# Optimization experiments

Measured on AMD Instinct MI355X. Metric: run time of the kernel, lower is better.

## Reference

```python
import jax, jax.numpy as jnp
import numpy as np

B, N, C, H, W = 2, 512, 32, 200, 200
THRESH = 0.05
# BEVCamera: x_range=y_range=(-1,1) -> FoV=2 meters; sh = H/FoVy = 100, sw = W/FoVx = 100
SH = H / 2.0
SW = W / 2.0
LOWPASS = 0.3        # 3DGS low-pass filter added to 2D cov diagonal
ALPHA_MIN = 1.0 / 255.0
ALPHA_MAX = 0.99


def setup_inputs() -> dict:
    key = jax.random.key(0)
    k1, k2, k3, k4 = jax.random.split(key, 4)
    features = jax.random.normal(k1, (B, N, C), dtype=jnp.float32)
    means3D = jax.random.uniform(k2, (B, N, 3), dtype=jnp.float32, minval=-1.0, maxval=1.0)
    # build PSD 3D covariances: Sigma = A A^T + eps*I, store 6 upper-tri entries
    A = 0.05 * jax.random.normal(k3, (B, N, 3, 3), dtype=jnp.float32)
    S = jnp.einsum('bnij,bnkj->bnik', A, A) + 1e-4 * jnp.eye(3, dtype=jnp.float32)
    cov3D = jnp.stack([S[..., 0, 0], S[..., 0, 1], S[..., 0, 2],
                       S[..., 1, 1], S[..., 1, 2], S[..., 2, 2]], axis=-1)
    opacities = jax.random.uniform(k4, (B, N, 1), dtype=jnp.float32)
    return {"features": features, "means3D": means3D, "cov3D": cov3D, "opacities": opacities}


def _render_one(features, means3D, cov3D, op):
    # features [N,C], means3D [N,3], cov3D [N,6] (xx,xy,xz,yy,yz,zz), op [N,1]
    dtype = features.dtype
    opac = op[:, 0]
    opac = jnp.where(opac > THRESH, opac, 0.0)  # masked-out gaussians contribute nothing
    # projmatrix: u = H/2 - sh*y (height), v = W/2 - sw*x (width)
    mu_u = H / 2.0 - SH * means3D[:, 1]
    mu_v = W / 2.0 - SW * means3D[:, 0]
    # 2D covariance from orthographic BEV projection J = [[0,-sh,0],[-sw,0,0]]
    Cuu = SH * SH * cov3D[:, 3] + LOWPASS
    Cvv = SW * SW * cov3D[:, 0] + LOWPASS
    Cuv = SH * SW * cov3D[:, 1]
    det = Cuu * Cvv - Cuv * Cuv
    valid = det > 0.0
    inv_det = jnp.where(valid, 1.0 / jnp.where(valid, det, 1.0), 0.0)
    Iuu = Cvv * inv_det
    Ivv = Cuu * inv_det
    Iuv = -Cuv * inv_det
    opac = jnp.where(valid, opac, 0.0)
    uu = jnp.arange(H, dtype=dtype)
    vv = jnp.arange(W, dtype=dtype)
    du = uu[None, :, None] - mu_u[:, None, None]   # [N,H,1]
    dv = vv[None, None, :] - mu_v[:, None, None]   # [N,1,W]
    power = (-0.5 * (Iuu[:, None, None] * du * du + Ivv[:, None, None] * dv * dv)
             - Iuv[:, None, None] * du * dv)       # [N,H,W]
    alpha = jnp.minimum(ALPHA_MAX, opac[:, None, None] * jnp.exp(jnp.minimum(power, 0.0)))
    alpha = jnp.where((power > 0.0) | (alpha < ALPHA_MIN), 0.0, alpha)
    # front-to-back alpha compositing in gaussian index order (all depths are 0 -> stable sort)
    logt = jnp.log1p(-alpha)                       # [N,H,W]
    T = jnp.exp(jnp.cumsum(logt, axis=0) - logt)   # exclusive transmittance
    w = T * alpha                                  # [N,H,W]
    return jnp.einsum('nhw,nc->chw', w, features)  # bg color is zeros


def reference(features, means3D, cov3D, opacities):
    bev = jax.vmap(_render_one)(features, means3D, cov3D, opacities)  # [B,C,H,W]
    num_gaussians = (opacities[..., 0] > THRESH).astype(jnp.float32).sum(axis=-1).mean()
    return bev, num_gaussians
```

## Files before the change

kernel.cpp:

```cpp
#include <hip/hip_runtime.h>
#include <math.h>

#define B_ 2
#define N_ 512
#define C_ 32
#define H_ 200
#define W_ 200
#define HW_ (H_*W_)
#define THRESH_ 0.05f
#define OUT_BEV (B_*C_*H_*W_)
#define NSEG 8
#define TILES_PER_B 625
#define LOG2E 1.4426950408889634f
#define LN2   0.6931471805599453f

__device__ inline float rlane(float x, int l) {
    return __int_as_float(__builtin_amdgcn_readlane(__float_as_int(x), l));
}

__global__ __launch_bounds__(512, 4) void render_kernel(
    const float* __restrict__ features,
    const float* __restrict__ means3D,
    const float* __restrict__ cov3D,
    const float* __restrict__ opacities,
    float* __restrict__ out)
{
    __shared__ float s_T[NSEG][64];
    __shared__ float s_W[NSEG * 64];
    __shared__ float s_acc[NSEG][NSEG][64];

    int blk = blockIdx.x;
    int tid = threadIdx.x;

    if (blk == B_ * TILES_PER_B) {
        float op0 = opacities[tid];
        float op1 = opacities[N_ + tid];
        int cnt = (op0 > THRESH_ ? 1 : 0) + (op1 > THRESH_ ? 1 : 0);
        for (int off = 32; off > 0; off >>= 1) cnt += __shfl_down(cnt, off);
        int* s_red = (int*)s_W;
        if ((tid & 63) == 0) s_red[tid >> 6] = cnt;
        __syncthreads();
        if (tid == 0) {
            int tot = 0;
            for (int g = 0; g < NSEG; ++g) tot += s_red[g];
            out[OUT_BEV] = (float)tot * 0.5f;
        }
        return;
    }

    int b  = blk / TILES_PER_B;
    int t  = blk - b * TILES_PER_B;
    int tu = t / 25;
    int tv = t - tu * 25;
    int wave = __builtin_amdgcn_readfirstlane(tid >> 6);
    int lane = tid & 63;

    float g_mu_u, g_mu_v, g_a2, g_b2, g_c2, g_op, g_thr2;
    bool ov;
    {
        int i = b * N_ + wave * 64 + lane;
        float x  = means3D[i*3 + 0];
        float y  = means3D[i*3 + 1];
        float c0 = cov3D[i*6 + 0];
        float c1 = cov3D[i*6 + 1];
        float c3 = cov3D[i*6 + 3];
        float op = opacities[i];
        g_mu_u = 100.0f - 100.0f * y;
        g_mu_v = 100.0f - 100.0f * x;
        float Cuu = 10000.0f * c3 + 0.3f;
        float Cvv = 10000.0f * c0 + 0.3f;
        float Cuv = 10000.0f * c1;
        float det = Cuu * Cvv - Cuv * Cuv;
        bool valid = det > 0.0f;
        float opac = (op > THRESH_) ? op : 0.0f;
        if (!valid) opac = 0.0f;
        float inv_det = valid ? (1.0f / det) : 0.0f;
        g_a2 = -0.5f * LOG2E * (Cvv * inv_det);
        g_b2 = -0.5f * LOG2E * (Cuu * inv_det);
        g_c2 =  LOG2E * (Cuv * inv_det);
        g_op = opac;
        float tu0 = (float)(tu * 8), tu1 = tu0 + 7.0f;
        float tv0 = (float)(tv * 8), tv1 = tv0 + 7.0f;
        if (opac > 0.0f) {
            float r2 = log2f(255.0f * opac);
            g_thr2 = -r2;
            float rn = LN2 * r2;
            float du_max = sqrtf(fmaxf(2.0f * rn * Cuu, 0.0f)) + 1.0e-3f;
            float dv_max = sqrtf(fmaxf(2.0f * rn * Cvv, 0.0f)) + 1.0e-3f;
            ov = (g_mu_u - du_max <= tu1) & (g_mu_u + du_max >= tu0) &
                 (g_mu_v - dv_max <= tv1) & (g_mu_v + dv_max >= tv0);
        } else {
            g_thr2 = 3.0e38f;
            ov = false;
        }
    }
    unsigned long long mask = __ballot(ov);

    int uu = tu * 8 + (lane >> 3);
    int vv = tv * 8 + (lane & 7);
    float u = (float)uu, v = (float)vv;

    float T = 1.0f;
    float acc[C_];
#pragma unroll
    for (int c = 0; c < C_; ++c) acc[c] = 0.0f;
    const float* featB = features + (size_t)b * (N_ * C_);
    int base_n = wave * 64;

    while (mask) {
        int j = __builtin_ctzll(mask);
        mask &= (mask - 1);
        float qmu_u = rlane(g_mu_u, j);
        float qmu_v = rlane(g_mu_v, j);
        float qa    = rlane(g_a2,   j);
        float qb    = rlane(g_b2,   j);
        float qc    = rlane(g_c2,   j);
        float qop   = rlane(g_op,   j);
        float qthr  = rlane(g_thr2, j);
        int n = base_n + j;
        const float* f = featB + (size_t)n * C_;
        float du = u - qmu_u;
        float dv = v - qmu_v;
        float pw = fmaf(qa * du, du, fmaf(qb * dv, dv, qc * (du * dv)));
        bool hit = (pw <= 0.0f) && (pw >= qthr);
        if (__any(hit)) {
            float al = hit ? fminf(0.99f, qop * exp2f(pw)) : 0.0f;
            float w  = T * al;
#pragma unroll
            for (int c = 0; c < C_; ++c) acc[c] = fmaf(w, f[c], acc[c]);
            T *= (1.0f - al);
        }
    }

    s_T[wave][lane] = T;
    __syncthreads();

    {
        float Wg = 1.0f;
        for (int gp = 0; gp < wave; ++gp) Wg *= s_T[gp][lane];
        s_W[wave * 64 + lane] = Wg;
    }

    size_t obase = (size_t)b * C_ * HW_ + (size_t)(tu * 8) * W_ + (size_t)(tv * 8);
#pragma unroll
    for (int k = 0; k < 4; ++k) {
#pragma unroll
        for (int c = 0; c < 8; ++c) s_acc[wave][c][lane] = acc[k * 8 + c];
        __syncthreads();
        float val = 0.0f;
#pragma unroll
        for (int g = 0; g < NSEG; ++g)
            val = fmaf(s_W[g * 64 + lane], s_acc[g][wave][lane], val);
        int c = k * 8 + wave;
        out[obase + (size_t)c * HW_ + (size_t)(lane >> 3) * W_ + (lane & 7)] = val;
        if (k < 3) __syncthreads();
    }
}

extern "C" void kernel_launch(void* const* d_in, const int* in_sizes, int n_in,
                              void* d_out, int out_size, void* d_ws, size_t ws_size,
                              hipStream_t stream) {
    const float* features  = (const float*)d_in[0];
    const float* means3D   = (const float*)d_in[1];
    const float* cov3D     = (const float*)d_in[2];
    const float* opacities = (const float*)d_in[3];
    float* out = (float*)d_out;
    render_kernel<<<B_ * TILES_PER_B + 1, 512, 0, stream>>>(
        features, means3D, cov3D, opacities, out);
}
```

Before: 17.29 us.

## Halve block size with 128 gaussians per wave and pairwise compositing

Result: faster. 16.91 us (-2.2%).

```diff
diff --git a/kernel.cpp b/kernel.cpp
--- a/kernel.cpp
+++ b/kernel.cpp
@@ -9,16 +9,91 @@
 #define HW_ (H_*W_)
 #define THRESH_ 0.05f
 #define OUT_BEV (B_*C_*H_*W_)
-#define NSEG 8
+#define NSEG 4
 #define TILES_PER_B 625
 #define LOG2E 1.4426950408889634f
 #define LN2   0.6931471805599453f
 
-__device__ inline float rlane(float x, int l) {
+__device__ __forceinline__ float rlane(float x, int l) {
     return __int_as_float(__builtin_amdgcn_readlane(__float_as_int(x), l));
 }
 
-__global__ __launch_bounds__(512, 4) void render_kernel(
+__device__ __forceinline__ bool pcompute(
+    const float* __restrict__ m3, const float* __restrict__ cv,
+    const float* __restrict__ opc, int i,
+    float tu0, float tu1, float tv0, float tv1,
+    float& mu_u, float& mu_v, float& a2, float& b2, float& c2,
+    float& opo, float& thr2)
+{
+    float x  = m3[i*3 + 0];
+    float y  = m3[i*3 + 1];
+    float c0 = cv[i*6 + 0];
+    float c1 = cv[i*6 + 1];
+    float c3 = cv[i*6 + 3];
+    float op = opc[i];
+    mu_u = 100.0f - 100.0f * y;
+    mu_v = 100.0f - 100.0f * x;
+    float Cuu = 10000.0f * c3 + 0.3f;
+    float Cvv = 10000.0f * c0 + 0.3f;
+    float Cuv = 10000.0f * c1;
+    float det = Cuu * Cvv - Cuv * Cuv;
+    bool valid = det > 0.0f;
+    float opac = (op > THRESH_) ? op : 0.0f;
+    if (!valid) opac = 0.0f;
+    float inv_det = valid ? (1.0f / det) : 0.0f;
+    a2 = -0.5f * LOG2E * (Cvv * inv_det);
+    b2 = -0.5f * LOG2E * (Cuu * inv_det);
+    c2 =  LOG2E * (Cuv * inv_det);
+    opo = opac;
+    if (opac > 0.0f) {
+        float r2 = log2f(255.0f * opac);
+        thr2 = -r2;
+        float rn = LN2 * r2;
+        float du_max = sqrtf(fmaxf(2.0f * rn * Cuu, 0.0f)) + 1.0e-3f;
+        float dv_max = sqrtf(fmaxf(2.0f * rn * Cvv, 0.0f)) + 1.0e-3f;
+        return (mu_u - du_max <= tu1) & (mu_u + du_max >= tu0) &
+               (mu_v - dv_max <= tv1) & (mu_v + dv_max >= tv0);
+    }
+    thr2 = 3.0e38f;
+    return false;
+}
+
+#define WALK(mask, P, base_n)                                                \
+    while (mask) {                                                           \
+        int j0 = __builtin_ctzll(mask); mask &= mask - 1;                    \
+        bool two = (mask != 0ull);                                           \
+        int j1 = two ? __builtin_ctzll(mask) : j0;                           \
+        if (two) mask &= mask - 1;                                           \
+        float mu_u0 = rlane(P##_mu_u, j0), mu_v0 = rlane(P##_mu_v, j0);      \
+        float a0 = rlane(P##_a, j0), b0 = rlane(P##_b, j0);                  \
+        float c0 = rlane(P##_c, j0), op0 = rlane(P##_op, j0);                \
+        float th0 = rlane(P##_th, j0);                                       \
+        float mu_u1 = rlane(P##_mu_u, j1), mu_v1 = rlane(P##_mu_v, j1);      \
+        float a1 = rlane(P##_a, j1), b1 = rlane(P##_b, j1);                  \
+        float c1 = rlane(P##_c, j1), op1 = rlane(P##_op, j1);                \
+        float th1 = rlane(P##_th, j1);                                       \
+        const float* f0 = featB + (size_t)((base_n) + j0) * C_;              \
+        const float* f1 = featB + (size_t)((base_n) + j1) * C_;              \
+        float du0 = u - mu_u0, dv0 = v - mu_v0;                              \
+        float pw0 = fmaf(a0 * du0, du0, fmaf(b0 * dv0, dv0, c0 * (du0 * dv0))); \
+        bool hit0 = (pw0 <= 0.0f) && (pw0 >= th0);                           \
+        float al0 = hit0 ? fminf(0.99f, op0 * exp2f(pw0)) : 0.0f;            \
+        float du1 = u - mu_u1, dv1 = v - mu_v1;                              \
+        float pw1 = fmaf(a1 * du1, du1, fmaf(b1 * dv1, dv1, c1 * (du1 * dv1))); \
+        bool hit1 = two && (pw1 <= 0.0f) && (pw1 >= th1);                    \
+        float al1 = hit1 ? fminf(0.99f, op1 * exp2f(pw1)) : 0.0f;            \
+        if (__any(hit0 | hit1)) {                                            \
+            float w0 = T * al0;                                              \
+            float Tm = T * (1.0f - al0);                                     \
+            float w1 = Tm * al1;                                             \
+            T = Tm * (1.0f - al1);                                           \
+            _Pragma("unroll")                                                \
+            for (int c = 0; c < C_; ++c)                                     \
+                acc[c] = fmaf(w1, f1[c], fmaf(w0, f0[c], acc[c]));           \
+        }                                                                    \
+    }
+
+__global__ __launch_bounds__(256, 5) void render_kernel(
     const float* __restrict__ features,
     const float* __restrict__ means3D,
     const float* __restrict__ cov3D,
@@ -27,24 +102,22 @@
 {
     __shared__ float s_T[NSEG][64];
     __shared__ float s_W[NSEG * 64];
-    __shared__ float s_acc[NSEG][NSEG][64];
+    __shared__ float s_acc[NSEG][8][64];
 
     int blk = blockIdx.x;
     int tid = threadIdx.x;
 
     if (blk == B_ * TILES_PER_B) {
-        float op0 = opacities[tid];
-        float op1 = opacities[N_ + tid];
-        int cnt = (op0 > THRESH_ ? 1 : 0) + (op1 > THRESH_ ? 1 : 0);
+        int cnt = ((opacities[tid]       > THRESH_) ? 1 : 0)
+                + ((opacities[tid + 256] > THRESH_) ? 1 : 0)
+                + ((opacities[tid + 512] > THRESH_) ? 1 : 0)
+                + ((opacities[tid + 768] > THRESH_) ? 1 : 0);
         for (int off = 32; off > 0; off >>= 1) cnt += __shfl_down(cnt, off);
         int* s_red = (int*)s_W;
         if ((tid & 63) == 0) s_red[tid >> 6] = cnt;
         __syncthreads();
-        if (tid == 0) {
-            int tot = 0;
-            for (int g = 0; g < NSEG; ++g) tot += s_red[g];
-            out[OUT_BEV] = (float)tot * 0.5f;
-        }
+        if (tid == 0)
+            out[OUT_BEV] = (float)(s_red[0] + s_red[1] + s_red[2] + s_red[3]) * 0.5f;
         return;
     }
 
@@ -55,46 +128,18 @@
     int wave = __builtin_amdgcn_readfirstlane(tid >> 6);
     int lane = tid & 63;
 
-    float g_mu_u, g_mu_v, g_a2, g_b2, g_c2, g_op, g_thr2;
-    bool ov;
-    {
-        int i = b * N_ + wave * 64 + lane;
-        float x  = means3D[i*3 + 0];
-        float y  = means3D[i*3 + 1];
-        float c0 = cov3D[i*6 + 0];
-        float c1 = cov3D[i*6 + 1];
-        float c3 = cov3D[i*6 + 3];
-        float op = opacities[i];
-        g_mu_u = 100.0f - 100.0f * y;
-        g_mu_v = 100.0f - 100.0f * x;
-        float Cuu = 10000.0f * c3 + 0.3f;
-        float Cvv = 10000.0f * c0 + 0.3f;
-        float Cuv = 10000.0f * c1;
-        float det = Cuu * Cvv - Cuv * Cuv;
-        bool valid = det > 0.0f;
-        float opac = (op > THRESH_) ? op : 0.0f;
-        if (!valid) opac = 0.0f;
-        float inv_det = valid ? (1.0f / det) : 0.0f;
-        g_a2 = -0.5f * LOG2E * (Cvv * inv_det);
-        g_b2 = -0.5f * LOG2E * (Cuu * inv_det);
-        g_c2 =  LOG2E * (Cuv * inv_det);
-        g_op = opac;
-        float tu0 = (float)(tu * 8), tu1 = tu0 + 7.0f;
-        float tv0 = (float)(tv * 8), tv1 = tv0 + 7.0f;
-        if (opac > 0.0f) {
-            float r2 = log2f(255.0f * opac);
-            g_thr2 = -r2;
-            float rn = LN2 * r2;
-            float du_max = sqrtf(fmaxf(2.0f * rn * Cuu, 0.0f)) + 1.0e-3f;
-            float dv_max = sqrtf(fmaxf(2.0f * rn * Cvv, 0.0f)) + 1.0e-3f;
-            ov = (g_mu_u - du_max <= tu1) & (g_mu_u + du_max >= tu0) &
-                 (g_mu_v - dv_max <= tv1) & (g_mu_v + dv_max >= tv0);
-        } else {
-            g_thr2 = 3.0e38f;
-            ov = false;
-        }
-    }
-    unsigned long long mask = __ballot(ov);
+    float tu0 = (float)(tu * 8), tu1 = tu0 + 7.0f;
+    float tv0 = (float)(tv * 8), tv1 = tv0 + 7.0f;
+
+    float A_mu_u, A_mu_v, A_a, A_b, A_c, A_op, A_th;
+    float B_mu_u, B_mu_v, B_a, B_b, B_c, B_op, B_th;
+    int i0 = b * N_ + wave * 128 + lane;
+    bool ovA = pcompute(means3D, cov3D, opacities, i0,      tu0, tu1, tv0, tv1,
+                        A_mu_u, A_mu_v, A_a, A_b, A_c, A_op, A_th);
+    bool ovB = pcompute(means3D, cov3D, opacities, i0 + 64, tu0, tu1, tv0, tv1,
+                        B_mu_u, B_mu_v, B_a, B_b, B_c, B_op, B_th);
+    unsigned long long m0 = __ballot(ovA);
+    unsigned long long m1 = __ballot(ovB);
 
     int uu = tu * 8 + (lane >> 3);
     int vv = tv * 8 + (lane & 7);
@@ -105,54 +150,35 @@
 #pragma unroll
     for (int c = 0; c < C_; ++c) acc[c] = 0.0f;
     const float* featB = features + (size_t)b * (N_ * C_);
-    int base_n = wave * 64;
 
-    while (mask) {
-        int j = __builtin_ctzll(mask);
-        mask &= (mask - 1);
-        float qmu_u = rlane(g_mu_u, j);
-        float qmu_v = rlane(g_mu_v, j);
-        float qa    = rlane(g_a2,   j);
-        float qb    = rlane(g_b2,   j);
-        float qc    = rlane(g_c2,   j);
-        float qop   = rlane(g_op,   j);
-        float qthr  = rlane(g_thr2, j);
-        int n = base_n + j;
-        const float* f = featB + (size_t)n * C_;
-        float du = u - qmu_u;
-        float dv = v - qmu_v;
-        float pw = fmaf(qa * du, du, fmaf(qb * dv, dv, qc * (du * dv)));
-        bool hit = (pw <= 0.0f) && (pw >= qthr);
-        if (__any(hit)) {
-            float al = hit ? fminf(0.99f, qop * exp2f(pw)) : 0.0f;
-            float w  = T * al;
-#pragma unroll
-            for (int c = 0; c < C_; ++c) acc[c] = fmaf(w, f[c], acc[c]);
-            T *= (1.0f - al);
-        }
-    }
+    WALK(m0, A, wave * 128)
+    WALK(m1, B, wave * 128 + 64)
 
     s_T[wave][lane] = T;
     __syncthreads();
 
     {
         float Wg = 1.0f;
-        for (int gp = 0; gp < wave; ++gp) Wg *= s_T[gp][lane];
+        for (int g = 0; g < wave; ++g) Wg *= s_T[g][lane];
         s_W[wave * 64 + lane] = Wg;
     }
 
     size_t obase = (size_t)b * C_ * HW_ + (size_t)(tu * 8) * W_ + (size_t)(tv * 8);
+    size_t opix  = (size_t)(lane >> 3) * W_ + (lane & 7);
 #pragma unroll
     for (int k = 0; k < 4; ++k) {
 #pragma unroll
-        for (int c = 0; c < 8; ++c) s_acc[wave][c][lane] = acc[k * 8 + c];
+        for (int cc = 0; cc < 8; ++cc) s_acc[wave][cc][lane] = acc[k * 8 + cc];
         __syncthreads();
-        float val = 0.0f;
+        float v0 = 0.0f, v1 = 0.0f;
 #pragma unroll
-        for (int g = 0; g < NSEG; ++g)
-            val = fmaf(s_W[g * 64 + lane], s_acc[g][wave][lane], val);
-        int c = k * 8 + wave;
-        out[obase + (size_t)c * HW_ + (size_t)(lane >> 3) * W_ + (lane & 7)] = val;
+        for (int g = 0; g < NSEG; ++g) {
+            float wgt = s_W[g * 64 + lane];
+            v0 = fmaf(wgt, s_acc[g][wave][lane],     v0);
+            v1 = fmaf(wgt, s_acc[g][wave + 4][lane], v1);
+        }
+        out[obase + (size_t)(k * 8 + wave) * HW_ + opix]     = v0;
+        out[obase + (size_t)(k * 8 + wave + 4) * HW_ + opix] = v1;
         if (k < 3) __syncthreads();
     }
 }
@@ -165,6 +191,6 @@
     const float* cov3D     = (const float*)d_in[2];
     const float* opacities = (const float*)d_in[3];
     float* out = (float*)d_out;
-    render_kernel<<<B_ * TILES_PER_B + 1, 512, 0, stream>>>(
+    render_kernel<<<B_ * TILES_PER_B + 1, 256, 0, stream>>>(
         features, means3D, cov3D, opacities, out);
 }
```

## Process three tiles per block and compact hit Gaussians into LDS

Applied to the files above, without the earlier changes.

New measurement: 21.19 us. +22.6%, slower.

```diff
diff --git a/kernel.cpp b/kernel.cpp
--- a/kernel.cpp
+++ b/kernel.cpp
@@ -10,13 +10,13 @@
 #define THRESH_ 0.05f
 #define OUT_BEV (B_*C_*H_*W_)
 #define NSEG 8
+#define TPB 3
+#define BPB 209
 #define TILES_PER_B 625
 #define LOG2E 1.4426950408889634f
 #define LN2   0.6931471805599453f
 
-__device__ inline float rlane(float x, int l) {
-    return __int_as_float(__builtin_amdgcn_readlane(__float_as_int(x), l));
-}
+typedef float v2f __attribute__((ext_vector_type(2)));
 
 __global__ __launch_bounds__(512, 4) void render_kernel(
     const float* __restrict__ features,
@@ -27,15 +27,16 @@
 {
     __shared__ float s_T[NSEG][64];
     __shared__ float s_W[NSEG * 64];
-    __shared__ float s_acc[NSEG][NSEG][64];
+    __shared__ float4 u_mem[NSEG * 16 * 16];
+    float4* s_hit = u_mem;
+    float (*s_acc)[16][64] = (float (*)[16][64])u_mem;
 
     int blk = blockIdx.x;
     int tid = threadIdx.x;
 
-    if (blk == B_ * TILES_PER_B) {
-        float op0 = opacities[tid];
-        float op1 = opacities[N_ + tid];
-        int cnt = (op0 > THRESH_ ? 1 : 0) + (op1 > THRESH_ ? 1 : 0);
+    if (blk == 2 * BPB) {
+        int cnt = ((opacities[tid]       > THRESH_) ? 1 : 0)
+                + ((opacities[tid + 512] > THRESH_) ? 1 : 0);
         for (int off = 32; off > 0; off >>= 1) cnt += __shfl_down(cnt, off);
         int* s_red = (int*)s_W;
         if ((tid & 63) == 0) s_red[tid >> 6] = cnt;
@@ -48,15 +49,12 @@
         return;
     }
 
-    int b  = blk / TILES_PER_B;
-    int t  = blk - b * TILES_PER_B;
-    int tu = t / 25;
-    int tv = t - tu * 25;
+    int b  = blk / BPB;
+    int tb = blk - b * BPB;
     int wave = __builtin_amdgcn_readfirstlane(tid >> 6);
     int lane = tid & 63;
 
-    float g_mu_u, g_mu_v, g_a2, g_b2, g_c2, g_op, g_thr2;
-    bool ov;
+    float mu_u, mu_v, a2, b2, c2, opac, thr2, du_max, dv_max;
     {
         int i = b * N_ + wave * 64 + lane;
         float x  = means3D[i*3 + 0];
@@ -65,95 +63,115 @@
         float c1 = cov3D[i*6 + 1];
         float c3 = cov3D[i*6 + 3];
         float op = opacities[i];
-        g_mu_u = 100.0f - 100.0f * y;
-        g_mu_v = 100.0f - 100.0f * x;
+        mu_u = 100.0f - 100.0f * y;
+        mu_v = 100.0f - 100.0f * x;
         float Cuu = 10000.0f * c3 + 0.3f;
         float Cvv = 10000.0f * c0 + 0.3f;
         float Cuv = 10000.0f * c1;
         float det = Cuu * Cvv - Cuv * Cuv;
         bool valid = det > 0.0f;
-        float opac = (op > THRESH_) ? op : 0.0f;
+        opac = (op > THRESH_) ? op : 0.0f;
         if (!valid) opac = 0.0f;
         float inv_det = valid ? (1.0f / det) : 0.0f;
-        g_a2 = -0.5f * LOG2E * (Cvv * inv_det);
-        g_b2 = -0.5f * LOG2E * (Cuu * inv_det);
-        g_c2 =  LOG2E * (Cuv * inv_det);
-        g_op = opac;
+        a2 = -0.5f * LOG2E * (Cvv * inv_det);
+        b2 = -0.5f * LOG2E * (Cuu * inv_det);
+        c2 =  LOG2E * (Cuv * inv_det);
+        if (opac > 0.0f) {
+            float r2 = log2f(255.0f * opac);
+            thr2 = -r2;
+            float rn = LN2 * r2;
+            du_max = sqrtf(fmaxf(2.0f * rn * Cuu, 0.0f)) + 1.0e-3f;
+            dv_max = sqrtf(fmaxf(2.0f * rn * Cvv, 0.0f)) + 1.0e-3f;
+        } else {
+            thr2 = 3.0e38f;
+            du_max = -1.0e30f;
+            dv_max = -1.0e30f;
+        }
+    }
+    const float* featB = features + (size_t)b * (N_ * C_);
+
+    for (int s = 0; s < TPB; ++s) {
+        int t = tb * TPB + s;
+        if (t >= TILES_PER_B) break;
+        int tu = t / 25;
+        int tv = t - tu * 25;
         float tu0 = (float)(tu * 8), tu1 = tu0 + 7.0f;
         float tv0 = (float)(tv * 8), tv1 = tv0 + 7.0f;
-        if (opac > 0.0f) {
-            float r2 = log2f(255.0f * opac);
-            g_thr2 = -r2;
-            float rn = LN2 * r2;
-            float du_max = sqrtf(fmaxf(2.0f * rn * Cuu, 0.0f)) + 1.0e-3f;
-            float dv_max = sqrtf(fmaxf(2.0f * rn * Cvv, 0.0f)) + 1.0e-3f;
-            ov = (g_mu_u - du_max <= tu1) & (g_mu_u + du_max >= tu0) &
-                 (g_mu_v - dv_max <= tv1) & (g_mu_v + dv_max >= tv0);
-        } else {
-            g_thr2 = 3.0e38f;
-            ov = false;
+
+        bool ov = (mu_u - du_max <= tu1) & (mu_u + du_max >= tu0) &
+                  (mu_v - dv_max <= tv1) & (mu_v + dv_max >= tv0);
+        unsigned long long m = __ballot(ov);
+        int pos = __builtin_amdgcn_mbcnt_hi((unsigned)(m >> 32),
+                  __builtin_amdgcn_mbcnt_lo((unsigned)m, 0));
+        if (ov) {
+            int sl = wave * 128 + 2 * pos;
+            s_hit[sl]     = make_float4(mu_u, mu_v, a2, b2);
+            s_hit[sl + 1] = make_float4(c2, opac, thr2, 0.0f);
         }
-    }
-    unsigned long long mask = __ballot(ov);
+        int nh = __builtin_amdgcn_readfirstlane(__popcll(m));
 
-    int uu = tu * 8 + (lane >> 3);
-    int vv = tv * 8 + (lane & 7);
-    float u = (float)uu, v = (float)vv;
+        int uu = tu * 8 + (lane >> 3);
+        int vv = tv * 8 + (lane & 7);
+        float u = (float)uu, v = (float)vv;
 
-    float T = 1.0f;
-    float acc[C_];
+        float T = 1.0f;
+        v2f acc2[16];
 #pragma unroll
-    for (int c = 0; c < C_; ++c) acc[c] = 0.0f;
-    const float* featB = features + (size_t)b * (N_ * C_);
-    int base_n = wave * 64;
+        for (int i = 0; i < 16; ++i) acc2[i] = (v2f){0.0f, 0.0f};
 
-    while (mask) {
-        int j = __builtin_ctzll(mask);
-        mask &= (mask - 1);
-        float qmu_u = rlane(g_mu_u, j);
-        float qmu_v = rlane(g_mu_v, j);
-        float qa    = rlane(g_a2,   j);
-        float qb    = rlane(g_b2,   j);
-        float qc    = rlane(g_c2,   j);
-        float qop   = rlane(g_op,   j);
-        float qthr  = rlane(g_thr2, j);
-        int n = base_n + j;
-        const float* f = featB + (size_t)n * C_;
-        float du = u - qmu_u;
-        float dv = v - qmu_v;
-        float pw = fmaf(qa * du, du, fmaf(qb * dv, dv, qc * (du * dv)));
-        bool hit = (pw <= 0.0f) && (pw >= qthr);
-        if (__any(hit)) {
-            float al = hit ? fminf(0.99f, qop * exp2f(pw)) : 0.0f;
-            float w  = T * al;
+        unsigned long long w = m;
+#pragma unroll 2
+        for (int k = 0; k < nh; ++k) {
+            float4 q0 = s_hit[wave * 128 + 2 * k];
+            float4 q1 = s_hit[wave * 128 + 2 * k + 1];
+            int j = __builtin_ctzll(w);
+            w &= w - 1;
+            int n = __builtin_amdgcn_readfirstlane(wave * 64 + j);
+            const v2f* f2 = (const v2f*)(featB + (size_t)n * C_);
+            float du = u - q0.x;
+            float dv = v - q0.y;
+            float pw = fmaf(q0.z * du, du, fmaf(q0.w * dv, dv, q1.x * (du * dv)));
+            bool hit = (pw <= 0.0f) && (pw >= q1.z);
+            float al = hit ? fminf(0.99f, q1.y * exp2f(pw)) : 0.0f;
+            float wgt = T * al;
+            v2f w2 = {wgt, wgt};
 #pragma unroll
-            for (int c = 0; c < C_; ++c) acc[c] = fmaf(w, f[c], acc[c]);
+            for (int i = 0; i < 16; ++i)
+                acc2[i] = __builtin_elementwise_fma(w2, f2[i], acc2[i]);
             T *= (1.0f - al);
         }
-    }
 
-    s_T[wave][lane] = T;
-    __syncthreads();
+        s_T[wave][lane] = T;
+        __syncthreads();
 
-    {
-        float Wg = 1.0f;
-        for (int gp = 0; gp < wave; ++gp) Wg *= s_T[gp][lane];
-        s_W[wave * 64 + lane] = Wg;
-    }
+        {
+            float Wg = 1.0f;
+            for (int g = 0; g < wave; ++g) Wg *= s_T[g][lane];
+            s_W[wave * 64 + lane] = Wg;
+        }
 
-    size_t obase = (size_t)b * C_ * HW_ + (size_t)(tu * 8) * W_ + (size_t)(tv * 8);
+        size_t obase = (size_t)b * C_ * HW_ + (size_t)(tu * 8) * W_ + (size_t)(tv * 8);
+        size_t opix  = (size_t)(lane >> 3) * W_ + (lane & 7);
 #pragma unroll
-    for (int k = 0; k < 4; ++k) {
+        for (int k2 = 0; k2 < 2; ++k2) {
 #pragma unroll
-        for (int c = 0; c < 8; ++c) s_acc[wave][c][lane] = acc[k * 8 + c];
-        __syncthreads();
-        float val = 0.0f;
+            for (int cc = 0; cc < 8; ++cc) {
+                v2f a = acc2[k2 * 8 + cc];
+                s_acc[wave][cc * 2][lane]     = a.x;
+                s_acc[wave][cc * 2 + 1][lane] = a.y;
+            }
+            __syncthreads();
+            float v0 = 0.0f, v1 = 0.0f;
 #pragma unroll
-        for (int g = 0; g < NSEG; ++g)
-            val = fmaf(s_W[g * 64 + lane], s_acc[g][wave][lane], val);
-        int c = k * 8 + wave;
-        out[obase + (size_t)c * HW_ + (size_t)(lane >> 3) * W_ + (lane & 7)] = val;
-        if (k < 3) __syncthreads();
+            for (int g = 0; g < NSEG; ++g) {
+                float wgt = s_W[g * 64 + lane];
+                v0 = fmaf(wgt, s_acc[g][wave * 2][lane],     v0);
+                v1 = fmaf(wgt, s_acc[g][wave * 2 + 1][lane], v1);
+            }
+            out[obase + (size_t)(k2 * 16 + wave * 2) * HW_ + opix]     = v0;
+            out[obase + (size_t)(k2 * 16 + wave * 2 + 1) * HW_ + opix] = v1;
+            __syncthreads();
+        }
     }
 }
 
@@ -165,6 +183,6 @@
     const float* cov3D     = (const float*)d_in[2];
     const float* opacities = (const float*)d_in[3];
     float* out = (float*)d_out;
-    render_kernel<<<B_ * TILES_PER_B + 1, 512, 0, stream>>>(
+    render_kernel<<<2 * BPB + 1, 512, 0, stream>>>(
         features, means3D, cov3D, opacities, out);
 }
```
